# Kernel tuning notes

Hardware: AMD Instinct MI355X
Metric: run time of the kernel (lower is better)

Reference implementation:

```python
import jax, jax.numpy as jnp
import numpy as np

B = 4; IMG = 32; P = 2; CIN = 3; G = IMG // P; N = G * G; D = 768; NL = 8
DI = 1536; NH = 24; HD = 64; DS = 128; CONVDIM = DI + 2 * DS; DPROJ = 2 * DI + 2 * DS + NH
OUTC = 3 * CIN; FREQ = 256; EPS = 1e-6


def _sincos_1d(dim, pos):
    omega = np.arange(dim // 2, dtype=np.float64) / (dim / 2.0)
    omega = 1.0 / 10000 ** omega
    out = np.einsum('m,d->md', pos.reshape(-1), omega)
    return np.concatenate([np.sin(out), np.cos(out)], axis=1)


def _pos_embed_2d(dim, gs):
    gh = np.arange(gs, dtype=np.float32)
    gw = np.arange(gs, dtype=np.float32)
    grid = np.stack(np.meshgrid(gw, gh), axis=0)
    return np.concatenate([_sincos_1d(dim // 2, grid[0]), _sincos_1d(dim // 2, grid[1])], axis=1)


POS = jnp.asarray(_pos_embed_2d(D, G), dtype=jnp.float32)[None]  # [1, N, D]


def _ln(x):
    m = x.mean(-1, keepdims=True)
    v = ((x - m) ** 2).mean(-1, keepdims=True)
    return (x - m) * jax.lax.rsqrt(v + EPS)


def _patch_embed(img, w, b):
    # conv with kernel=stride=P == reshape to (c, ph, pw)-ordered patch vectors + matmul
    xp = img.reshape(B, CIN, G, P, G, P).transpose(0, 2, 4, 1, 3, 5).reshape(B, N, CIN * P * P)
    return xp @ w + b


def _t_embed(t, tw1, tb1, tw2, tb2):
    half = FREQ // 2
    freqs = jnp.exp(-jnp.log(10000.0) * jnp.arange(half, dtype=jnp.float32) / half)
    args = t[:, None] * freqs[None]
    emb = jnp.concatenate([jnp.cos(args), jnp.sin(args)], axis=-1)
    return jax.nn.silu(emb @ tw1 + tb1) @ tw2 + tb2


def _mamba2(u, in_w, conv_w, conv_b, dt_bias, A_log, D_ssm, out_w):
    # u: [B, N, D]
    zxbcdt = u @ in_w                           # [B, N, DPROJ]
    z = zxbcdt[..., :DI]
    xBC = zxbcdt[..., DI:DI + CONVDIM]
    dt_raw = zxbcdt[..., DI + CONVDIM:]
    # causal depthwise conv1d, kernel 4
    pad = jnp.pad(xBC, ((0, 0), (3, 0), (0, 0)))
    xBC = sum(pad[:, k:k + N, :] * conv_w[:, k] for k in range(4)) + conv_b
    xBC = jax.nn.silu(xBC)
    xs = xBC[..., :DI].reshape(B, N, NH, HD)
    Bm = xBC[..., DI:DI + DS]
    Cm = xBC[..., DI + DS:]
    dt = jax.nn.softplus(dt_raw + dt_bias)       # [B, N, NH]
    a = dt * (-jnp.exp(A_log))                   # [B, N, NH], negative
    acum = jnp.cumsum(a, axis=1)
    seg = acum[:, :, None, :] - acum[:, None, :, :]   # [B, l, s, NH]
    tril = jnp.tril(jnp.ones((N, N), bool))
    decay = jnp.exp(jnp.where(tril[None, :, :, None], seg, -1e30))
    decay = jnp.moveaxis(decay, -1, 1)           # [B, NH, l, s]
    CB = jnp.einsum('bln,bsn->bls', Cm, Bm)
    scores = CB[:, None] * decay * jnp.moveaxis(dt, -1, 1)[:, :, None, :]
    y = jnp.einsum('bhls,bshp->blhp', scores, xs) + D_ssm[None, None, :, None] * xs
    y = y.reshape(B, N, DI) * jax.nn.silu(z)
    return y @ out_w


def _conv3(x, w, b):
    o = jax.lax.conv_general_dilated(x, w, (1, 1), 'SAME',
                                     dimension_numbers=('NCHW', 'OIHW', 'NCHW'))
    return o + b[None, :, None, None]


def _hfnet(h, w1, b1, w2, b2, w3, b3):
    c = jax.nn.relu(_conv3(h, w1, b1))
    c = jax.nn.relu(_conv3(c, w2, b2))
    return h + _conv3(c, w3, b3)


def _forward(x, t, y, H1, H2, H3, xe_w, xe_b, ye_w, ye_b, tw1, tb1, tw2, tb2,
             adaln_w, adaln_b, in_w, conv_w, conv_b, dt_bias, A_log, D_ssm, out_w,
             fl_t_w, fl_t_b, fl_y_w, fl_y_b, fl_lin_w, fl_lin_b,
             e1_w1, e1_b1, e1_w2, e1_b2, e1_w3, e1_b3,
             e2_w1, e2_b1, e2_w2, e2_b2, e2_w3, e2_b3,
             e3_w1, e3_b1, e3_w2, e3_b2, e3_w3, e3_b3):
    xe = _patch_embed(x, xe_w, xe_b) + POS
    ye = _patch_embed(y, ye_w, ye_b) + POS
    te = _t_embed(t, tw1, tb1, tw2, tb2)
    st = jax.nn.silu(te)          # [B, D]
    sy = jax.nn.silu(ye)          # [B, N, D]

    def layer(xc, p):
        aw, ab, iw, cw, cb, db, al, dd, ow = p
        sh_t, sc_t, g_t = jnp.split(st @ aw + ab, 3, axis=-1)
        sh_y, sc_y, g_y = jnp.split(sy @ aw + ab, 3, axis=-1)
        shift = sh_t[:, None] + sh_y
        scale = sc_t[:, None] + sc_y
        gate = g_t[:, None] + g_y
        xm = _ln(xc) * (1.0 + scale) + shift
        return gate * _mamba2(xm, iw, cw, cb, db, al, dd, ow) + xc, None

    xh, _ = jax.lax.scan(layer, xe, (adaln_w, adaln_b, in_w, conv_w, conv_b,
                                     dt_bias, A_log, D_ssm, out_w))
    sh_t, sc_t = jnp.split(st @ fl_t_w + fl_t_b, 2, axis=-1)
    sh_y, sc_y = jnp.split(sy @ fl_y_w + fl_y_b, 2, axis=-1)
    xf = (_ln(xh) * (1.0 + sc_t[:, None] + sc_y) + sh_t[:, None] + sh_y) @ fl_lin_w + fl_lin_b
    # unpatchify: nhwpqc -> nchpwq
    img = xf.reshape(B, G, G, P, P, OUTC).transpose(0, 5, 1, 3, 2, 4).reshape(B, OUTC, IMG, IMG)
    h1 = _hfnet(H1, e1_w1, e1_b1, e1_w2, e1_b2, e1_w3, e1_b3)
    h2 = _hfnet(H2, e2_w1, e2_b1, e2_w2, e2_b2, e2_w3, e2_b3)
    h3 = _hfnet(H3, e3_w1, e3_b1, e3_w2, e3_b2, e3_w3, e3_b3)
    return (img, h1, h2, h3)


def setup_inputs() -> dict:
    ks = iter(jax.random.split(jax.random.key(0), 80))
    def nrm(shape, s=0.02):
        return jax.random.normal(next(ks), shape, jnp.float32) * s
    z = lambda *s: jnp.zeros(s, jnp.float32)
    inp = {}
    inp['x'] = jax.random.normal(next(ks), (B, CIN, IMG, IMG), jnp.float32)
    inp['t'] = jax.random.uniform(next(ks), (B,), jnp.float32) * 1000.0
    inp['y'] = jax.random.normal(next(ks), (B, CIN, IMG, IMG), jnp.float32)
    inp['H1'] = jax.random.normal(next(ks), (B, CIN, IMG, IMG), jnp.float32)
    inp['H2'] = jax.random.normal(next(ks), (B, CIN, IMG, IMG), jnp.float32)
    inp['H3'] = jax.random.normal(next(ks), (B, CIN, IMG, IMG), jnp.float32)
    inp['xe_w'] = nrm((CIN * P * P, D), 0.1); inp['xe_b'] = z(D)
    inp['ye_w'] = nrm((CIN * P * P, D), 0.1); inp['ye_b'] = z(D)
    inp['tw1'] = nrm((FREQ, D)); inp['tb1'] = z(D)
    inp['tw2'] = nrm((D, D)); inp['tb2'] = z(D)
    inp['adaln_w'] = nrm((NL, D, 3 * D)); inp['adaln_b'] = nrm((NL, 3 * D))
    inp['in_w'] = nrm((NL, D, DPROJ))
    inp['conv_w'] = nrm((NL, CONVDIM, 4), 0.2); inp['conv_b'] = z(NL, CONVDIM)
    inp['dt_bias'] = nrm((NL, NH), 0.5)
    inp['A_log'] = jnp.tile(jnp.log(jnp.arange(1.0, NH + 1.0, dtype=jnp.float32)), (NL, 1))
    inp['D_ssm'] = jnp.ones((NL, NH), jnp.float32)
    inp['out_w'] = nrm((NL, DI, D))
    inp['fl_t_w'] = nrm((D, 2 * D)); inp['fl_t_b'] = z(2 * D)
    inp['fl_y_w'] = nrm((D, 2 * D)); inp['fl_y_b'] = z(2 * D)
    inp['fl_lin_w'] = nrm((D, P * P * OUTC)); inp['fl_lin_b'] = z(P * P * OUTC)
    for i in (1, 2, 3):
        inp['e%d_w1' % i] = nrm((64, CIN, 3, 3), 0.1); inp['e%d_b1' % i] = z(64)
        inp['e%d_w2' % i] = nrm((64, 64, 3, 3), 0.05); inp['e%d_b2' % i] = z(64)
        inp['e%d_w3' % i] = nrm((CIN, 64, 3, 3), 0.05); inp['e%d_b3' % i] = z(CIN)
    return inp


def reference(x, t, y, H1, H2, H3, xe_w, xe_b, ye_w, ye_b, tw1, tb1, tw2, tb2,
              adaln_w, adaln_b, in_w, conv_w, conv_b, dt_bias, A_log, D_ssm, out_w,
              fl_t_w, fl_t_b, fl_y_w, fl_y_b, fl_lin_w, fl_lin_b,
              e1_w1, e1_b1, e1_w2, e1_b2, e1_w3, e1_b3,
              e2_w1, e2_b1, e2_w2, e2_b2, e2_w3, e2_b3,
              e3_w1, e3_b1, e3_w2, e3_b2, e3_w3, e3_b3):
    return _forward(x, t, y, H1, H2, H3, xe_w, xe_b, ye_w, ye_b, tw1, tb1, tw2, tb2,
                    adaln_w, adaln_b, in_w, conv_w, conv_b, dt_bias, A_log, D_ssm, out_w,
                    fl_t_w, fl_t_b, fl_y_w, fl_y_b, fl_lin_w, fl_lin_b,
                    e1_w1, e1_b1, e1_w2, e1_b2, e1_w3, e1_b3,
                    e2_w1, e2_b1, e2_w2, e2_b2, e2_w3, e2_b3,
                    e3_w1, e3_b1, e3_w2, e3_b2, e3_w3, e3_b3)
```

## Files before the change

### kernel.cpp

```cpp
#include <hip/hip_runtime.h>
#include <cmath>

namespace {

constexpr int kB = 4;
constexpr int kN = 256;
constexpr int kD = 768;
constexpr int kNL = 8;
constexpr int kDI = 1536;
constexpr int kNH = 24;
constexpr int kHD = 64;
constexpr int kCONV = 1792;
constexpr int kDPROJ = 3352;
constexpr int kD3 = 2304;
constexpr int kNCAT = 19968;
constexpr int kOFF_FL = 18432;

typedef __attribute__((ext_vector_type(8))) short short8;
typedef __attribute__((ext_vector_type(4))) short short4v;
typedef __attribute__((ext_vector_type(4))) float f32x4;

__device__ __forceinline__ float siluf(float x) { return x / (1.f + expf(-x)); }

__device__ __forceinline__ short f2bf(float f) {
  unsigned u = __float_as_uint(f);
  unsigned r = (u + 0x7fffu + ((u >> 16) & 1u)) >> 16;
  return (short)r;
}

__device__ __forceinline__ void gload_lds16(const void* g, void* l) {
  __builtin_amdgcn_global_load_lds(
      (const __attribute__((address_space(1))) void*)g,
      (__attribute__((address_space(3))) void*)l, 16, 0, 0);
}

template <int N> __device__ __forceinline__ void wait_barrier();
template <> __device__ __forceinline__ void wait_barrier<0>() {
  asm volatile("s_waitcnt vmcnt(0)\n\ts_barrier" ::: "memory");
}
template <> __device__ __forceinline__ void wait_barrier<2>() {
  asm volatile("s_waitcnt vmcnt(2)\n\ts_barrier" ::: "memory");
}
template <> __device__ __forceinline__ void wait_barrier<3>() {
  asm volatile("s_waitcnt vmcnt(3)\n\ts_barrier" ::: "memory");
}
template <> __device__ __forceinline__ void wait_barrier<4>() {
  asm volatile("s_waitcnt vmcnt(4)\n\ts_barrier" ::: "memory");
}

__global__ void patch_embed2_kernel(const float* __restrict__ img0,
                                    const float* __restrict__ w0,
                                    const float* __restrict__ b0,
                                    float* __restrict__ out0,
                                    const float* __restrict__ img1,
                                    const float* __restrict__ w1,
                                    const float* __restrict__ b1,
                                    float* __restrict__ out1,
                                    short* __restrict__ out1_bf) {
  int gid = blockIdx.x * blockDim.x + threadIdx.x;
  if (gid >= kB * kN * kD) return;
  int z = blockIdx.z;
  const float* img = z ? img1 : img0;
  const float* w = z ? w1 : w0;
  const float* bias = z ? b1 : b0;
  int d = gid % kD;
  int n = (gid / kD) % kN;
  int b = gid / (kD * kN);
  int gi = n >> 4, gj = n & 15;
  float acc = bias[d];
#pragma unroll
  for (int c = 0; c < 3; ++c)
#pragma unroll
    for (int pi = 0; pi < 2; ++pi)
#pragma unroll
      for (int pj = 0; pj < 2; ++pj) {
        float v = img[((b * 3 + c) * 32 + gi * 2 + pi) * 32 + gj * 2 + pj];
        acc += v * w[(c * 4 + pi * 2 + pj) * kD + d];
      }
  float pos;
  if (d < 192)       pos = sinf((float)gj * powf(10000.f, -(float)d / 192.f));
  else if (d < 384)  pos = cosf((float)gj * powf(10000.f, -(float)(d - 192) / 192.f));
  else if (d < 576)  pos = sinf((float)gi * powf(10000.f, -(float)(d - 384) / 192.f));
  else               pos = cosf((float)gi * powf(10000.f, -(float)(d - 576) / 192.f));
  acc += pos;
  if (z) {
    float v = siluf(acc);
    out1[gid] = v;
    out1_bf[gid] = f2bf(v);
  } else {
    out0[gid] = acc;
  }
}

__global__ void tembed_args_kernel(const float* __restrict__ t,
                                   float* __restrict__ ctst) {
  int idx = blockIdx.x * 256 + threadIdx.x;
  if (idx >= kB * 256) return;
  int b = idx >> 8, j = idx & 255;
  int k = j & 127;
  float f = expf(-9.210340371976184f * (float)k / 128.f);
  float arg = t[b] * f;
  ctst[idx] = (j < 128) ? cosf(arg) : sinf(arg);
}

__global__ __launch_bounds__(256) void splitk_mm_stage1(
    const float* __restrict__ A, const float* __restrict__ W,
    float* __restrict__ part, int K, int Nn, int KC) {
  int n = blockIdx.x * 256 + threadIdx.x;
  int kc = blockIdx.y;
  int l = blockIdx.z;
  if (n >= Nn) return;
  const float* w = W + (size_t)l * K * Nn + (size_t)kc * 64 * Nn + n;
  int kb = kc * 64;
  float a0 = 0.f, a1 = 0.f, a2 = 0.f, a3 = 0.f;
  for (int k = 0; k < 64; ++k) {
    float wv = w[(size_t)k * Nn];
    a0 += A[0 * K + kb + k] * wv;
    a1 += A[1 * K + kb + k] * wv;
    a2 += A[2 * K + kb + k] * wv;
    a3 += A[3 * K + kb + k] * wv;
  }
  size_t base = (((size_t)l * KC + kc) * 4) * Nn + n;
  part[base] = a0;
  part[base + Nn] = a1;
  part[base + 2 * (size_t)Nn] = a2;
  part[base + 3 * (size_t)Nn] = a3;
}

__global__ void splitk_mm_reduce(const float* __restrict__ part,
                                 const float* __restrict__ bias,
                                 float* __restrict__ C, int Nn, int KC, int L,
                                 int act) {
  int idx = blockIdx.x * 256 + threadIdx.x;
  if (idx >= L * 4 * Nn) return;
  int n = idx % Nn;
  int b = (idx / Nn) & 3;
  int l = idx / (4 * Nn);
  float s = bias[(size_t)l * Nn + n];
  for (int kc = 0; kc < KC; ++kc)
    s += part[(((size_t)l * KC + kc) * 4 + b) * Nn + n];
  C[idx] = act ? siluf(s) : s;
}

__global__ __launch_bounds__(256) void transposeW_kernel(
    const float* __restrict__ W, short* __restrict__ Wt, int K, int N,
    size_t sW, size_t sWt) {
  W += (size_t)blockIdx.z * sW;
  Wt += (size_t)blockIdx.z * sWt;
  __shared__ float tile[32][33];
  int n0 = blockIdx.x * 32, k0 = blockIdx.y * 32;
  int tid = threadIdx.x;
  int tx = tid & 31, ty = tid >> 5;
#pragma unroll
  for (int i = 0; i < 4; ++i) {
    int k = k0 + ty + i * 8;
    int n = n0 + tx;
    tile[ty + i * 8][tx] = (n < N) ? W[(size_t)k * N + n] : 0.f;
  }
  __syncthreads();
#pragma unroll
  for (int i = 0; i < 4; ++i) {
    int n = n0 + ty + i * 8;
    int k = k0 + tx;
    Wt[(size_t)n * K + k] = f2bf(tile[tx][ty + i * 8]);
  }
}

__global__ void concat_bias_kernel(const float* __restrict__ a,
                                   const float* __restrict__ b,
                                   float* __restrict__ dst) {
  int i = blockIdx.x * 256 + threadIdx.x;
  if (i < kOFF_FL) dst[i] = a[i];
  else if (i < kNCAT) dst[i] = b[i - kOFF_FL];
}

template <int BM, int BN>
__global__ __launch_bounds__(256) void mfma_gemm(
    const short* __restrict__ A, const short* __restrict__ Bt,
    const float* __restrict__ bias, float* __restrict__ C,
    int Nn, int Ksplit, int Ktot, int ldc, size_t czstride) {
  constexpr int MI = BM / 32;
  constexpr int NJ = BN / 32;
  constexpr int LPW = BM / 64 + BN / 64;
  __shared__ short Als[3 * BM * 32];
  __shared__ short Bls[3 * BN * 32];
  int gx = gridDim.x, gy = gridDim.y;
  int nblk = gx * gy;
  int hl = blockIdx.y * gx + blockIdx.x;
  int txi, tyi;
  if ((nblk & 7) == 0) {
    int chunk = nblk >> 3;
    int s_id = (hl & 7) * chunk + (hl >> 3);
    txi = s_id / gy;
    tyi = s_id % gy;
  } else {
    txi = blockIdx.x;
    tyi = blockIdx.y;
  }
  int m0 = tyi * BM, n0 = txi * BN;
  int koff = blockIdx.z * Ksplit;
  C += (size_t)blockIdx.z * czstride;
  int tid = threadIdx.x;
  int lane = tid & 63, wid = tid >> 6;
  int wr = wid >> 1, wc = wid & 1;
  f32x4 acc[MI][NJ] = {};
  int sm = tid >> 2;
  int sk = (tid & 3) * 8;
  const int nsteps = Ksplit >> 5;
  auto stage = [&](int buf, int k0) {
#pragma unroll
    for (int h = 0; h < BM / 64; ++h)
      gload_lds16(&A[(size_t)(m0 + h * 64 + sm) * Ktot + koff + k0 + sk],
                  &Als[buf * (BM * 32) + h * 2048 + wid * 512]);
#pragma unroll
    for (int h = 0; h < BN / 64; ++h)
      gload_lds16(&Bt[(size_t)(n0 + h * 64 + sm) * Ktot + koff + k0 + sk],
                  &Bls[buf * (BN * 32) + h * 2048 + wid * 512]);
  };
  stage(0, 0);
  if (nsteps > 1) stage(1, 32);
  int cur = 0;
  for (int s = 0; s < nsteps; ++s) {
    if (s + 1 < nsteps) wait_barrier<LPW>();
    else wait_barrier<0>();
    if (s + 2 < nsteps) stage(cur == 0 ? 2 : cur - 1, (s + 2) << 5);
    short8 av[MI], bv[NJ];
#pragma unroll
    for (int mi = 0; mi < MI; ++mi)
      av[mi] = *(const short8*)&Als[cur * (BM * 32) +
                                    (wr * (BM / 2) + mi * 16 + (lane & 15)) *
                                        32 +
                                    (lane >> 4) * 8];
#pragma unroll
    for (int nj = 0; nj < NJ; ++nj)
      bv[nj] = *(const short8*)&Bls[cur * (BN * 32) +
                                    (wc * (BN / 2) + nj * 16 + (lane & 15)) *
                                        32 +
                                    (lane >> 4) * 8];
#pragma unroll
    for (int mi = 0; mi < MI; ++mi)
#pragma unroll
      for (int nj = 0; nj < NJ; ++nj)
        acc[mi][nj] = __builtin_amdgcn_mfma_f32_16x16x32_bf16(
            av[mi], bv[nj], acc[mi][nj], 0, 0, 0);
    cur = (cur == 2) ? 0 : cur + 1;
  }
#pragma unroll
  for (int mi = 0; mi < MI; ++mi)
#pragma unroll
    for (int nj = 0; nj < NJ; ++nj)
#pragma unroll
      for (int r = 0; r < 4; ++r) {
        int gm = m0 + wr * (BM / 2) + mi * 16 + (lane >> 4) * 4 + r;
        int gn = n0 + wc * (BN / 2) + nj * 16 + (lane & 15);
        if (gn >= Nn) continue;
        C[(size_t)gm * ldc + gn] = acc[mi][nj][r] + (bias ? bias[gn] : 0.f);
      }
}

__global__ __launch_bounds__(256) void ln_mod_kernel(
    const float* __restrict__ x, const float* __restrict__ tA,
    const float* __restrict__ yA, short* __restrict__ out_bf, int tstride,
    int ystride, const float* __restrict__ p0, const float* __restrict__ p1,
    const float* __restrict__ gtA, const float* __restrict__ gyA,
    float* __restrict__ xcw) {
  int row = blockIdx.x;
  int b = row >> 8;
  int tid = threadIdx.x;
  __shared__ float w1[4], w2[4];
  float xr[3];
  float s = 0.f;
#pragma unroll
  for (int k = 0; k < 3; ++k) {
    int i = tid + k * 256;
    float v = x[(size_t)row * kD + i];
    if (p0) {
      float g = gtA[b * kD3 + 2 * kD + i] +
                gyA[(size_t)row * kNCAT + 2 * kD + i];
      v += g * (p0[(size_t)row * kD + i] + p1[(size_t)row * kD + i]);
      xcw[(size_t)row * kD + i] = v;
    }
    xr[k] = v;
    s += v;
  }
#pragma unroll
  for (int o = 32; o > 0; o >>= 1) s += __shfl_down(s, o, 64);
  if ((tid & 63) == 0) w1[tid >> 6] = s;
  __syncthreads();
  float mean = (w1[0] + w1[1] + w1[2] + w1[3]) * (1.f / kD);
  float s2 = 0.f;
#pragma unroll
  for (int k = 0; k < 3; ++k) {
    float d = xr[k] - mean;
    s2 += d * d;
  }
#pragma unroll
  for (int o = 32; o > 0; o >>= 1) s2 += __shfl_down(s2, o, 64);
  if ((tid & 63) == 0) w2[tid >> 6] = s2;
  __syncthreads();
  float rstd = rsqrtf((w2[0] + w2[1] + w2[2] + w2[3]) * (1.f / kD) + 1e-6f);
#pragma unroll
  for (int k = 0; k < 3; ++k) {
    int i = tid + k * 256;
    float sc = tA[b * tstride + kD + i] + yA[(size_t)row * ystride + kD + i];
    float sh = tA[b * tstride + i] + yA[(size_t)row * ystride + i];
    float v = (xr[k] - mean) * rstd * (1.f + sc) + sh;
    out_bf[(size_t)row * kD + i] = f2bf(v);
  }
}

__global__ __launch_bounds__(256) void convdt_kernel(
    const float* __restrict__ zx, const float* __restrict__ cw,
    const float* __restrict__ cb, const float* __restrict__ db,
    const float* __restrict__ al, float* __restrict__ xbc,
    short* __restrict__ bB, short* __restrict__ bC, float* __restrict__ dts,
    float* __restrict__ acum) {
  constexpr int kC4 = kCONV / 4;
  constexpr int kConvBlocks = kB * kN * kC4 / 256;
  int blk = blockIdx.x;
  if (blk < kConvBlocks) {
    int idx = blk * 256 + threadIdx.x;
    int c4 = idx % kC4;
    int row = idx / kC4;
    int n = row & 255, b = row >> 8;
    int c0 = c4 * 4;
    float acc[4];
    {
      float4 bv = *(const float4*)&cb[c0];
      acc[0] = bv.x; acc[1] = bv.y; acc[2] = bv.z; acc[3] = bv.w;
    }
    float4 taps[4];
#pragma unroll
    for (int j = 0; j < 4; ++j) taps[j] = *(const float4*)&cw[(c0 + j) * 4];
#pragma unroll
    for (int k = 0; k < 4; ++k) {
      int ns = n + k - 3;
      if (ns < 0) continue;
      float4 v =
          *(const float4*)&zx[(size_t)(b * kN + ns) * kDPROJ + kDI + c0];
      acc[0] += v.x * ((const float*)&taps[0])[k];
      acc[1] += v.y * ((const float*)&taps[1])[k];
      acc[2] += v.z * ((const float*)&taps[2])[k];
      acc[3] += v.w * ((const float*)&taps[3])[k];
    }
    float4 outv;
    float* o = (float*)&outv;
#pragma unroll
    for (int j = 0; j < 4; ++j) o[j] = siluf(acc[j]);
    *(float4*)&xbc[(size_t)row * kCONV + c0] = outv;
    if (c0 >= kDI) {
      short4v sv;
#pragma unroll
      for (int j = 0; j < 4; ++j) sv[j] = f2bf(o[j]);
      if (c0 < kDI + 128)
        *(short4v*)&bB[(size_t)row * 128 + (c0 - kDI)] = sv;
      else
        *(short4v*)&bC[(size_t)row * 128 + (c0 - kDI - 128)] = sv;
    }
  } else {
    int bh = blk - kConvBlocks;
    int b = bh / kNH, h = bh % kNH;
    int n = threadIdx.x;
    __shared__ float sb[256];
    size_t row = (size_t)(b * kN + n);
    float xv = zx[row * kDPROJ + (kDI + kCONV) + h] + db[h];
    float dt = xv > 20.f ? xv : log1pf(expf(xv));
    dts[row * kNH + h] = dt;
    float a = -expf(al[h]) * dt;
    sb[n] = a;
    __syncthreads();
    for (int off = 1; off < 256; off <<= 1) {
      float v = (n >= off) ? sb[n - off] : 0.f;
      __syncthreads();
      sb[n] += v;
      __syncthreads();
    }
    acum[row * kNH + h] = sb[n];
  }
}

__global__ __launch_bounds__(256) void ssm_y_kernel(
    const short* __restrict__ bCm, const short* __restrict__ bBm,
    const float* __restrict__ acum, const float* __restrict__ dts,
    const float* __restrict__ xbc, const float* __restrict__ zx,
    const float* __restrict__ Dssm, short* __restrict__ ybuf) {
  int bh = blockIdx.z;
  int b = bh / kNH, h = bh % kNH;
  int m0 = blockIdx.y * 64;
  int tid = threadIdx.x;
  int lane = tid & 63, wid = tid >> 6;
  int tx = tid & 15, ty = tid >> 4;
  __shared__ float As[16][65];
  __shared__ float Xs[16][64];
  float acc[4][4] = {};
  float acum_l[4];
#pragma unroll
  for (int r = 0; r < 4; ++r) {
    int l = m0 + wid * 16 + (lane >> 4) * 4 + r;
    acum_l[r] = acum[(size_t)(b * kN + l) * kNH + h];
  }
  const short* cRow =
      &bCm[((size_t)(b * kN + m0 + wid * 16 + (lane & 15))) * 128 +
           (lane >> 4) * 8];
  for (int k0 = 0; k0 < kN; k0 += 16) {
    if (k0 > m0 + 63) break;
    f32x4 cb = {};
    const short* bRow =
        &bBm[((size_t)(b * kN + k0 + (lane & 15))) * 128 + (lane >> 4) * 8];
#pragma unroll
    for (int ks = 0; ks < 4; ++ks)
      cb = __builtin_amdgcn_mfma_f32_16x16x32_bf16(
          *(const short8*)(cRow + ks * 32), *(const short8*)(bRow + ks * 32),
          cb, 0, 0, 0);
    int ss = k0 + (lane & 15);
    float acum_ss = acum[(size_t)(b * kN + ss) * kNH + h];
    float dts_ss = dts[(size_t)(b * kN + ss) * kNH + h];
#pragma unroll
    for (int i = 0; i < 4; ++i) {
      int e = tid + i * 256;
      int k = e >> 6, n = e & 63;
      Xs[k][n] = xbc[(size_t)(b * kN + k0 + k) * kCONV + h * kHD + n];
    }
#pragma unroll
    for (int r = 0; r < 4; ++r) {
      int mloc = wid * 16 + (lane >> 4) * 4 + r;
      int l = m0 + mloc;
      float v = 0.f;
      if (ss <= l) v = cb[r] * expf(acum_l[r] - acum_ss) * dts_ss;
      As[lane & 15][mloc] = v;
    }
    __syncthreads();
#pragma unroll
    for (int kk = 0; kk < 16; ++kk) {
      float a[4], bb[4];
#pragma unroll
      for (int i = 0; i < 4; ++i) a[i] = As[kk][ty * 4 + i];
#pragma unroll
      for (int j = 0; j < 4; ++j) bb[j] = Xs[kk][tx * 4 + j];
#pragma unroll
      for (int i = 0; i < 4; ++i)
#pragma unroll
        for (int j = 0; j < 4; ++j) acc[i][j] += a[i] * bb[j];
    }
    __syncthreads();
  }
  float dd = Dssm[h];
#pragma unroll
  for (int i = 0; i < 4; ++i) {
    int l = m0 + ty * 4 + i;
    size_t row = (size_t)(b * kN + l);
#pragma unroll
    for (int j = 0; j < 4; ++j) {
      int p = tx * 4 + j;
      int col = h * kHD + p;
      float xs_l = xbc[row * kCONV + col];
      float yv = acc[i][j] + dd * xs_l;
      float zv = zx[row * kDPROJ + col];
      ybuf[row * kDI + col] = f2bf(yv * siluf(zv));
    }
  }
}

__global__ void unpatchify_kernel(const float* __restrict__ fpp,
                                  const float* __restrict__ bias,
                                  float* __restrict__ out) {
  constexpr int kFP = kB * kN * 36;
  int gid = blockIdx.x * 256 + threadIdx.x;
  if (gid >= kFP) return;
  int j = gid % 36;
  int row = gid / 36;
  int n = row & 255, b = row >> 8;
  int o = j % 9;
  int pj = (j / 9) & 1;
  int pi = j / 18;
  int gi = n >> 4, gj = n & 15;
  float v = fpp[gid] + fpp[kFP + gid] + fpp[2 * kFP + gid] +
            fpp[3 * kFP + gid] + bias[j];
  out[((b * 9 + o) * 32 + gi * 2 + pi) * 32 + (gj * 2 + pj)] = v;
}

__global__ __launch_bounds__(256) void conv1_kernel(
    const float* __restrict__ Ha, const float* __restrict__ Hb,
    const float* __restrict__ Hc, const float* __restrict__ wa,
    const float* __restrict__ wb, const float* __restrict__ wc,
    const float* __restrict__ ba, const float* __restrict__ bb,
    const float* __restrict__ bc, short* __restrict__ dst) {
  int gid = blockIdx.x * 256 + threadIdx.x;
  if (gid >= 3 * 4096 * 64) return;
  int oc = gid & 63;
  int px = (gid >> 6) & 4095;
  int net = gid >> 18;
  const float* in = net == 0 ? Ha : (net == 1 ? Hb : Hc);
  const float* w = net == 0 ? wa : (net == 1 ? wb : wc);
  const float* bs = net == 0 ? ba : (net == 1 ? bb : bc);
  int xx = px & 31, yy = (px >> 5) & 31, b = px >> 10;
  float acc = bs[oc];
#pragma unroll
  for (int ic = 0; ic < 3; ++ic) {
    const float* ip = in + ((size_t)(b * 3 + ic) << 10);
    const float* wp = w + (oc * 3 + ic) * 9;
#pragma unroll
    for (int ky = 0; ky < 3; ++ky) {
      int ys = yy + ky - 1;
      if (ys < 0 || ys > 31) continue;
#pragma unroll
      for (int kx = 0; kx < 3; ++kx) {
        int xs = xx + kx - 1;
        if (xs < 0 || xs > 31) continue;
        acc += ip[ys * 32 + xs] * wp[ky * 3 + kx];
      }
    }
  }
  dst[gid] = f2bf(fmaxf(acc, 0.f));
}

__global__ __launch_bounds__(256) void convw_prep_kernel(
    const float* __restrict__ w2a, const float* __restrict__ w2b,
    const float* __restrict__ w2c, const float* __restrict__ w3a,
    const float* __restrict__ w3b, const float* __restrict__ w3c,
    short* __restrict__ dst2, short* __restrict__ dst3) {
  int idx = blockIdx.x * 256 + threadIdx.x;
  if (idx >= 3 * 128 * 576) return;
  int z = blockIdx.z;
  int OC = z ? 3 : 64;
  short* dst = z ? dst3 : dst2;
  int k = idx % 576;
  int row = (idx / 576) & 127;
  int net = idx / (128 * 576);
  const float* w = z ? (net == 0 ? w3a : (net == 1 ? w3b : w3c))
                     : (net == 0 ? w2a : (net == 1 ? w2b : w2c));
  int pos = k >> 6, ic = k & 63;
  float v = (row < OC) ? w[row * 576 + ic * 9 + pos] : 0.f;
  dst[idx] = f2bf(v);
}

template <int EP>
__global__ __launch_bounds__(256) void conv_gemm(
    const short* __restrict__ src, const short* __restrict__ Btall,
    const float* __restrict__ b_a, const float* __restrict__ b_b,
    const float* __restrict__ b_c, const float* __restrict__ r_a,
    const float* __restrict__ r_b, const float* __restrict__ r_c,
    short* __restrict__ dst, float* __restrict__ outp) {
  constexpr int K = 576;
  __shared__ short Als[128 * 32];
  __shared__ short Bls[128 * 32];
  int net = blockIdx.z;
  int m0 = blockIdx.y * 128;
  const float* bias = net == 0 ? b_a : (net == 1 ? b_b : b_c);
  const float* res = net == 0 ? r_a : (net == 1 ? r_b : r_c);
  const short* Bt = Btall + (size_t)net * 128 * K;
  int tid = threadIdx.x;
  int lane = tid & 63, wid = tid >> 6;
  int wr = wid >> 1, wc = wid & 1;
  f32x4 acc[4][4] = {};
  int sm = tid >> 2;
  int sk = (tid & 3) * 8;
  for (int k0 = 0; k0 < K; k0 += 32) {
    int kk = k0 + sk;
    int pos = kk >> 6, ic0 = kk & 63;
    int ky = pos / 3 - 1, kx = pos % 3 - 1;
    uint4 a_st[2], b_st[2];
#pragma unroll
    for (int i = 0; i < 2; ++i) {
      int px = m0 + i * 64 + sm;
      int b = px >> 10;
      int yy = (px >> 5) & 31, xx = px & 31;
      int ys = yy + ky, xs = xx + kx;
      if (ys >= 0 && ys < 32 && xs >= 0 && xs < 32) {
        a_st[i] = *(const uint4*)&src[((size_t)(net * 4096 + (b << 10) +
                                                (ys << 5) + xs)
                                       << 6) +
                                      ic0];
      } else {
        a_st[i] = make_uint4(0u, 0u, 0u, 0u);
      }
      b_st[i] = *(const uint4*)&Bt[(size_t)(i * 64 + sm) * K + kk];
    }
    __syncthreads();
    *(uint4*)&Als[sm * 32 + sk] = a_st[0];
    *(uint4*)&Als[(64 + sm) * 32 + sk] = a_st[1];
    *(uint4*)&Bls[sm * 32 + sk] = b_st[0];
    *(uint4*)&Bls[(64 + sm) * 32 + sk] = b_st[1];
    __syncthreads();
    short8 av[4], bv[4];
#pragma unroll
    for (int mi = 0; mi < 4; ++mi)
      av[mi] = *(const short8*)&Als[(wr * 64 + mi * 16 + (lane & 15)) * 32 +
                                    (lane >> 4) * 8];
#pragma unroll
    for (int nj = 0; nj < 4; ++nj)
      bv[nj] = *(const short8*)&Bls[(wc * 64 + nj * 16 + (lane & 15)) * 32 +
                                    (lane >> 4) * 8];
#pragma unroll
    for (int mi = 0; mi < 4; ++mi)
#pragma unroll
      for (int nj = 0; nj < 4; ++nj)
        acc[mi][nj] = __builtin_amdgcn_mfma_f32_16x16x32_bf16(
            av[mi], bv[nj], acc[mi][nj], 0, 0, 0);
  }
#pragma unroll
  for (int mi = 0; mi < 4; ++mi)
#pragma unroll
    for (int nj = 0; nj < 4; ++nj)
#pragma unroll
      for (int r = 0; r < 4; ++r) {
        int gm = m0 + wr * 64 + mi * 16 + (lane >> 4) * 4 + r;
        int gn = wc * 64 + nj * 16 + (lane & 15);
        float v = acc[mi][nj][r];
        if (EP == 0) {
          if (gn < 64)
            dst[(size_t)(net * 4096 + gm) * 64 + gn] =
                f2bf(fmaxf(v + bias[gn], 0.f));
        } else {
          if (gn < 3) {
            int b = gm >> 10, pix = gm & 1023;
            size_t o = (size_t)(b * 3 + gn) * 1024 + pix;
            outp[36864 + net * 12288 + o] = v + bias[gn] + res[o];
          }
        }
      }
}

}

extern "C" void kernel_launch(void* const* d_in, const int* in_sizes, int n_in,
                              void* d_out, int out_size, void* d_ws,
                              size_t ws_size, hipStream_t stream) {
  const float* x = (const float*)d_in[0];
  const float* t = (const float*)d_in[1];
  const float* y = (const float*)d_in[2];
  const float* H[3] = {(const float*)d_in[3], (const float*)d_in[4],
                       (const float*)d_in[5]};
  const float* xe_w = (const float*)d_in[6];
  const float* xe_b = (const float*)d_in[7];
  const float* ye_w = (const float*)d_in[8];
  const float* ye_b = (const float*)d_in[9];
  const float* tw1 = (const float*)d_in[10];
  const float* tb1 = (const float*)d_in[11];
  const float* tw2 = (const float*)d_in[12];
  const float* tb2 = (const float*)d_in[13];
  const float* adaln_w = (const float*)d_in[14];
  const float* adaln_b = (const float*)d_in[15];
  const float* in_w = (const float*)d_in[16];
  const float* conv_w = (const float*)d_in[17];
  const float* conv_b = (const float*)d_in[18];
  const float* dt_bias = (const float*)d_in[19];
  const float* A_log = (const float*)d_in[20];
  const float* D_ssm = (const float*)d_in[21];
  const float* out_w = (const float*)d_in[22];
  const float* fl_t_w = (const float*)d_in[23];
  const float* fl_t_b = (const float*)d_in[24];
  const float* fl_y_w = (const float*)d_in[25];
  const float* fl_y_b = (const float*)d_in[26];
  const float* fl_lin_w = (const float*)d_in[27];
  const float* fl_lin_b = (const float*)d_in[28];

  float* out = (float*)d_out;
  float* ws = (float*)d_ws;

  size_t off = 0;
  auto alloc = [&](size_t nelem) { float* p = ws + off; off += nelem; return p; };
  float* xc    = alloc((size_t)kB * kN * kD);
  float* sy    = alloc((size_t)kB * kN * kD);
  short* sy_bf = (short*)alloc((size_t)kB * kN * kD / 2);
  float* st    = alloc((size_t)kB * kD);
  float* ht    = alloc((size_t)kB * kD);
  float* ctst  = alloc((size_t)kB * 256);
  float* tAall = alloc((size_t)kNL * kB * kD3);
  float* yA8   = alloc((size_t)kB * kN * kNCAT);
  short* xm_bf = (short*)alloc((size_t)kB * kN * kD / 2);
  float* zx    = alloc((size_t)kB * kN * kDPROJ);
  float* xbc   = alloc((size_t)kB * kN * kCONV);
  float* dts   = alloc((size_t)kB * kN * kNH);
  float* acum  = alloc((size_t)kB * kN * kNH);
  short* ybuf  = (short*)alloc((size_t)kB * kN * kDI / 2);
  float* tfl   = alloc((size_t)kB * 2 * kD);
  float* opart = alloc((size_t)2 * kB * kN * kD);
  float* fpp   = alloc((size_t)4 * kB * kN * 36);
  short* adalnT = (short*)alloc((size_t)kNCAT * kD / 2);
  float* biascat = alloc(kNCAT);
  short* in_wT = (short*)alloc((size_t)kNL * 3456 * kD / 2);
  short* Wt    = (short*)alloc((size_t)128 * kD / 2);
  short* bBm   = (short*)alloc((size_t)kB * kN * 128 / 2);
  short* bCm   = (short*)alloc((size_t)kB * kN * 128 / 2);
  short* c1bf  = (short*)alloc((size_t)3 * 4096 * 64 / 2);
  short* c2bf  = (short*)alloc((size_t)3 * 4096 * 64 / 2);
  short* Bt2   = (short*)alloc((size_t)3 * 128 * 576 / 2);
  short* Bt3   = (short*)alloc((size_t)3 * 128 * 576 / 2);
  (void)ws_size;

  float* part = zx;
  short* out_wT = adalnT;

  dim3 blk(256);

  patch_embed2_kernel<<<dim3((kB * kN * kD + 255) / 256, 1, 2), blk, 0,
                        stream>>>(x, xe_w, xe_b, xc, y, ye_w, ye_b, sy, sy_bf);

  transposeW_kernel<<<dim3(72, 24, kNL), blk, 0, stream>>>(
      adaln_w, adalnT, kD, kD3, (size_t)kD * kD3, (size_t)kD3 * kD);
  transposeW_kernel<<<dim3(48, 24, 1), blk, 0, stream>>>(
      fl_y_w, adalnT + (size_t)kOFF_FL * kD, kD, 2 * kD, 0, 0);
  concat_bias_kernel<<<dim3((kNCAT + 255) / 256), blk, 0, stream>>>(
      adaln_b, fl_y_b, biascat);
  mfma_gemm<128, 128><<<dim3(kNCAT / 128, 8), blk, 0, stream>>>(
      sy_bf, adalnT, biascat, yA8, kNCAT, kD, kD, kNCAT, 0);

  transposeW_kernel<<<dim3(108, 24, kNL), blk, 0, stream>>>(
      in_w, in_wT, kD, kDPROJ, (size_t)kD * kDPROJ, (size_t)3456 * kD);
  transposeW_kernel<<<dim3(24, 48, kNL), blk, 0, stream>>>(
      out_w, out_wT, kDI, kD, (size_t)kDI * kD, (size_t)768 * kDI);

  tembed_args_kernel<<<dim3(4), blk, 0, stream>>>(t, ctst);
  splitk_mm_stage1<<<dim3(3, 4, 1), blk, 0, stream>>>(ctst, tw1, part, 256,
                                                      kD, 4);
  splitk_mm_reduce<<<dim3((kB * kD + 255) / 256), blk, 0, stream>>>(
      part, tb1, ht, kD, 4, 1, 1);
  splitk_mm_stage1<<<dim3(3, 12, 1), blk, 0, stream>>>(ht, tw2, part, kD, kD, 12);
  splitk_mm_reduce<<<dim3((kB * kD + 255) / 256), blk, 0, stream>>>(
      part, tb2, st, kD, 12, 1, 1);
  splitk_mm_stage1<<<dim3(9, 12, kNL), blk, 0, stream>>>(st, adaln_w, part, kD,
                                                         kD3, 12);
  splitk_mm_reduce<<<dim3((kNL * kB * kD3 + 255) / 256), blk, 0, stream>>>(
      part, adaln_b, tAall, kD3, 12, kNL, 0);
  splitk_mm_stage1<<<dim3(6, 12, 1), blk, 0, stream>>>(st, fl_t_w, part, kD,
                                                       2 * kD, 12);
  splitk_mm_reduce<<<dim3((kB * 2 * kD + 255) / 256), blk, 0, stream>>>(
      part, fl_t_b, tfl, 2 * kD, 12, 1, 0);

  for (int l = 0; l < kNL; ++l) {
    const float* cw = conv_w + (size_t)l * kCONV * 4;
    const float* cb = conv_b + (size_t)l * kCONV;
    const float* db = dt_bias + (size_t)l * kNH;
    const float* al = A_log + (size_t)l * kNH;
    const float* dd = D_ssm + (size_t)l * kNH;
    float* tA = tAall + (size_t)l * kB * kD3;
    const float* yAl = yA8 + (size_t)l * kD3;
    const float* ptA = l ? tAall + (size_t)(l - 1) * kB * kD3 : nullptr;
    const float* pyA = l ? yA8 + (size_t)(l - 1) * kD3 : nullptr;

    ln_mod_kernel<<<dim3(kB * kN), blk, 0, stream>>>(
        xc, tA, yAl, xm_bf, kD3, kNCAT, l ? opart : nullptr,
        l ? opart + (size_t)kB * kN * kD : nullptr, ptA, pyA, xc);
    mfma_gemm<64, 64><<<dim3(54, 16), blk, 0, stream>>>(
        xm_bf, in_wT + (size_t)l * 3456 * kD, nullptr, zx, kDPROJ, kD, kD,
        kDPROJ, 0);
    convdt_kernel<<<dim3(kB * kN * (kCONV / 4) / 256 + kB * kNH), blk, 0,
                    stream>>>(zx, cw, cb, db, al, xbc, bBm, bCm, dts, acum);
    ssm_y_kernel<<<dim3(1, kN / 64, kB * kNH), blk, 0, stream>>>(
        bCm, bBm, acum, dts, xbc, zx, dd, ybuf);
    mfma_gemm<64, 64><<<dim3(12, 16, 2), blk, 0, stream>>>(
        ybuf, out_wT + (size_t)l * 768 * kDI, nullptr, opart, kD, kD, kDI,
        kD, (size_t)kB * kN * kD);
  }

  ln_mod_kernel<<<dim3(kB * kN), blk, 0, stream>>>(
      xc, tfl, yA8 + kOFF_FL, xm_bf, 2 * kD, kNCAT, opart,
      opart + (size_t)kB * kN * kD, tAall + (size_t)7 * kB * kD3,
      yA8 + (size_t)7 * kD3, xc);
  transposeW_kernel<<<dim3(4, 24, 1), blk, 0, stream>>>(fl_lin_w, Wt, kD, 36,
                                                        0, 0);
  mfma_gemm<64, 128><<<dim3(1, 16, 4), blk, 0, stream>>>(
      xm_bf, Wt, nullptr, fpp, 36, 192, kD, 36, (size_t)kB * kN * 36);
  unpatchify_kernel<<<dim3((kB * kN * 36 + 255) / 256), blk, 0, stream>>>(
      fpp, fl_lin_b, out);

  const float* w1s[3] = {(const float*)d_in[29], (const float*)d_in[35],
                         (const float*)d_in[41]};
  const float* b1s[3] = {(const float*)d_in[30], (const float*)d_in[36],
                         (const float*)d_in[42]};
  const float* w2s[3] = {(const float*)d_in[31], (const float*)d_in[37],
                         (const float*)d_in[43]};
  const float* b2s[3] = {(const float*)d_in[32], (const float*)d_in[38],
                         (const float*)d_in[44]};
  const float* w3s[3] = {(const float*)d_in[33], (const float*)d_in[39],
                         (const float*)d_in[45]};
  const float* b3s[3] = {(const float*)d_in[34], (const float*)d_in[40],
                         (const float*)d_in[46]};
  convw_prep_kernel<<<dim3((3 * 128 * 576 + 255) / 256, 1, 2), blk, 0,
                      stream>>>(w2s[0], w2s[1], w2s[2], w3s[0], w3s[1],
                                w3s[2], Bt2, Bt3);
  conv1_kernel<<<dim3(3 * 4096 * 64 / 256), blk, 0, stream>>>(
      H[0], H[1], H[2], w1s[0], w1s[1], w1s[2], b1s[0], b1s[1], b1s[2], c1bf);
  conv_gemm<0><<<dim3(1, 32, 3), blk, 0, stream>>>(
      c1bf, Bt2, b2s[0], b2s[1], b2s[2], nullptr, nullptr, nullptr, c2bf,
      nullptr);
  conv_gemm<1><<<dim3(1, 32, 3), blk, 0, stream>>>(
      c2bf, Bt3, b3s[0], b3s[1], b3s[2], H[0], H[1], H[2], nullptr, out);
}
```

Before: 1.011 ms.

## Split-K the in-projection GEMM and deepen out-projection split-K

The in-projection GEMM now runs split-K over two halves of K, writing two partial buffers that the conv/dt and SSM output kernels sum on read. The out-projection split goes from two to four partials, which the LN-modulate kernel sums. The SSM kernel also reverses its row-block order so the heavier causal tiles are scheduled first. These changes raise block counts for GPU occupancy, at the cost of extra partial-buffer memory traffic and redundant partial reads.

```diff
diff --git a/kernel.cpp b/kernel.cpp
--- a/kernel.cpp
+++ b/kernel.cpp
@@ -261,7 +261,7 @@
 __global__ __launch_bounds__(256) void ln_mod_kernel(
     const float* __restrict__ x, const float* __restrict__ tA,
     const float* __restrict__ yA, short* __restrict__ out_bf, int tstride,
-    int ystride, const float* __restrict__ p0, const float* __restrict__ p1,
+    int ystride, const float* __restrict__ p0, size_t pstride,
     const float* __restrict__ gtA, const float* __restrict__ gyA,
     float* __restrict__ xcw) {
   int row = blockIdx.x;
@@ -277,8 +277,11 @@
     if (p0) {
       float g = gtA[b * kD3 + 2 * kD + i] +
                 gyA[(size_t)row * kNCAT + 2 * kD + i];
-      v += g * (p0[(size_t)row * kD + i] + p1[(size_t)row * kD + i]);
-      xcw[(size_t)row * kD + i] = v;
+      size_t o = (size_t)row * kD + i;
+      float ps = p0[o] + p0[o + pstride] + p0[o + 2 * pstride] +
+                 p0[o + 3 * pstride];
+      v += g * ps;
+      xcw[o] = v;
     }
     xr[k] = v;
     s += v;
@@ -310,11 +313,11 @@
 }
 
 __global__ __launch_bounds__(256) void convdt_kernel(
-    const float* __restrict__ zx, const float* __restrict__ cw,
-    const float* __restrict__ cb, const float* __restrict__ db,
-    const float* __restrict__ al, float* __restrict__ xbc,
-    short* __restrict__ bB, short* __restrict__ bC, float* __restrict__ dts,
-    float* __restrict__ acum) {
+    const float* __restrict__ zx0, const float* __restrict__ zx1,
+    const float* __restrict__ cw, const float* __restrict__ cb,
+    const float* __restrict__ db, const float* __restrict__ al,
+    float* __restrict__ xbc, short* __restrict__ bB, short* __restrict__ bC,
+    float* __restrict__ dts, float* __restrict__ acum) {
   constexpr int kC4 = kCONV / 4;
   constexpr int kConvBlocks = kB * kN * kC4 / 256;
   int blk = blockIdx.x;
@@ -336,12 +339,13 @@
     for (int k = 0; k < 4; ++k) {
       int ns = n + k - 3;
       if (ns < 0) continue;
-      float4 v =
-          *(const float4*)&zx[(size_t)(b * kN + ns) * kDPROJ + kDI + c0];
-      acc[0] += v.x * ((const float*)&taps[0])[k];
-      acc[1] += v.y * ((const float*)&taps[1])[k];
-      acc[2] += v.z * ((const float*)&taps[2])[k];
-      acc[3] += v.w * ((const float*)&taps[3])[k];
+      size_t o = (size_t)(b * kN + ns) * kDPROJ + kDI + c0;
+      float4 v0 = *(const float4*)&zx0[o];
+      float4 v1 = *(const float4*)&zx1[o];
+      acc[0] += (v0.x + v1.x) * ((const float*)&taps[0])[k];
+      acc[1] += (v0.y + v1.y) * ((const float*)&taps[1])[k];
+      acc[2] += (v0.z + v1.z) * ((const float*)&taps[2])[k];
+      acc[3] += (v0.w + v1.w) * ((const float*)&taps[3])[k];
     }
     float4 outv;
     float* o = (float*)&outv;
@@ -363,7 +367,8 @@
     int n = threadIdx.x;
     __shared__ float sb[256];
     size_t row = (size_t)(b * kN + n);
-    float xv = zx[row * kDPROJ + (kDI + kCONV) + h] + db[h];
+    size_t zo = row * kDPROJ + (kDI + kCONV) + h;
+    float xv = zx0[zo] + zx1[zo] + db[h];
     float dt = xv > 20.f ? xv : log1pf(expf(xv));
     dts[row * kNH + h] = dt;
     float a = -expf(al[h]) * dt;
@@ -382,11 +387,12 @@
 __global__ __launch_bounds__(256) void ssm_y_kernel(
     const short* __restrict__ bCm, const short* __restrict__ bBm,
     const float* __restrict__ acum, const float* __restrict__ dts,
-    const float* __restrict__ xbc, const float* __restrict__ zx,
-    const float* __restrict__ Dssm, short* __restrict__ ybuf) {
+    const float* __restrict__ xbc, const float* __restrict__ zx0,
+    const float* __restrict__ zx1, const float* __restrict__ Dssm,
+    short* __restrict__ ybuf) {
   int bh = blockIdx.z;
   int b = bh / kNH, h = bh % kNH;
-  int m0 = blockIdx.y * 64;
+  int m0 = (3 - blockIdx.y) * 64;
   int tid = threadIdx.x;
   int lane = tid & 63, wid = tid >> 6;
   int tx = tid & 15, ty = tid >> 4;
@@ -455,7 +461,8 @@
       int col = h * kHD + p;
       float xs_l = xbc[row * kCONV + col];
       float yv = acc[i][j] + dd * xs_l;
-      float zv = zx[row * kDPROJ + col];
+      size_t zo = row * kDPROJ + col;
+      float zv = zx0[zo] + zx1[zo];
       ybuf[row * kDI + col] = f2bf(yv * siluf(zv));
     }
   }
@@ -669,13 +676,13 @@
   float* tAall = alloc((size_t)kNL * kB * kD3);
   float* yA8   = alloc((size_t)kB * kN * kNCAT);
   short* xm_bf = (short*)alloc((size_t)kB * kN * kD / 2);
-  float* zx    = alloc((size_t)kB * kN * kDPROJ);
+  float* zx    = alloc((size_t)2 * kB * kN * kDPROJ);
   float* xbc   = alloc((size_t)kB * kN * kCONV);
   float* dts   = alloc((size_t)kB * kN * kNH);
   float* acum  = alloc((size_t)kB * kN * kNH);
   short* ybuf  = (short*)alloc((size_t)kB * kN * kDI / 2);
   float* tfl   = alloc((size_t)kB * 2 * kD);
-  float* opart = alloc((size_t)2 * kB * kN * kD);
+  float* opart = alloc((size_t)4 * kB * kN * kD);
   float* fpp   = alloc((size_t)4 * kB * kN * 36);
   short* adalnT = (short*)alloc((size_t)kNCAT * kD / 2);
   float* biascat = alloc(kNCAT);
@@ -690,6 +697,7 @@
   (void)ws_size;
 
   float* part = zx;
+  float* zx1 = zx + (size_t)kB * kN * kDPROJ;
   short* out_wT = adalnT;
 
   dim3 blk(256);
@@ -741,22 +749,23 @@
 
     ln_mod_kernel<<<dim3(kB * kN), blk, 0, stream>>>(
         xc, tA, yAl, xm_bf, kD3, kNCAT, l ? opart : nullptr,
-        l ? opart + (size_t)kB * kN * kD : nullptr, ptA, pyA, xc);
-    mfma_gemm<64, 64><<<dim3(54, 16), blk, 0, stream>>>(
-        xm_bf, in_wT + (size_t)l * 3456 * kD, nullptr, zx, kDPROJ, kD, kD,
-        kDPROJ, 0);
+        (size_t)kB * kN * kD, ptA, pyA, xc);
+    mfma_gemm<64, 64><<<dim3(54, 16, 2), blk, 0, stream>>>(
+        xm_bf, in_wT + (size_t)l * 3456 * kD, nullptr, zx, kDPROJ, 384, kD,
+        kDPROJ, (size_t)kB * kN * kDPROJ);
     convdt_kernel<<<dim3(kB * kN * (kCONV / 4) / 256 + kB * kNH), blk, 0,
-                    stream>>>(zx, cw, cb, db, al, xbc, bBm, bCm, dts, acum);
+                    stream>>>(zx, zx1, cw, cb, db, al, xbc, bBm, bCm, dts,
+                              acum);
     ssm_y_kernel<<<dim3(1, kN / 64, kB * kNH), blk, 0, stream>>>(
-        bCm, bBm, acum, dts, xbc, zx, dd, ybuf);
-    mfma_gemm<64, 64><<<dim3(12, 16, 2), blk, 0, stream>>>(
-        ybuf, out_wT + (size_t)l * 768 * kDI, nullptr, opart, kD, kD, kDI,
+        bCm, bBm, acum, dts, xbc, zx, zx1, dd, ybuf);
+    mfma_gemm<64, 64><<<dim3(12, 16, 4), blk, 0, stream>>>(
+        ybuf, out_wT + (size_t)l * 768 * kDI, nullptr, opart, kD, 384, kDI,
         kD, (size_t)kB * kN * kD);
   }
 
   ln_mod_kernel<<<dim3(kB * kN), blk, 0, stream>>>(
       xc, tfl, yA8 + kOFF_FL, xm_bf, 2 * kD, kNCAT, opart,
-      opart + (size_t)kB * kN * kD, tAall + (size_t)7 * kB * kD3,
+      (size_t)kB * kN * kD, tAall + (size_t)7 * kB * kD3,
       yA8 + (size_t)7 * kD3, xc);
   transposeW_kernel<<<dim3(4, 24, 1), blk, 0, stream>>>(fl_lin_w, Wt, kD, 36,
                                                         0, 0);
```

Result: slower. 1.068 ms (+5.7%).
